# Performance work log

Hardware: AMD Instinct MI355X
Metric: run time of the kernel (lower is better)

The kernel has to match this reference:

```python
import jax, jax.numpy as jnp
import numpy as np

D_MODEL = 1024
N_HEADS = 16
N_KV_HEADS = 4
HEAD_DIM = D_MODEL // N_HEADS
GROUP = N_HEADS // N_KV_HEADS
ROPE_BASE = 10000.0


def _rope(x):
    # x: (B, H, T, Dh); standard rotate-half RoPE, base 10000
    B, H, T, Dh = x.shape
    inv_freq = 1.0 / (ROPE_BASE ** (jnp.arange(0, Dh, 2, dtype=jnp.float32) / Dh))
    t = jnp.arange(T, dtype=jnp.float32)
    freqs = t[:, None] * inv_freq[None, :]              # (T, Dh/2)
    emb = jnp.concatenate([freqs, freqs], axis=-1)      # (T, Dh)
    cos = jnp.cos(emb)[None, None].astype(x.dtype)
    sin = jnp.sin(emb)[None, None].astype(x.dtype)
    x1, x2 = x[..., : Dh // 2], x[..., Dh // 2 :]
    rot = jnp.concatenate([-x2, x1], axis=-1)
    return x * cos + rot * sin


def setup_inputs() -> dict:
    key = jax.random.key(0)
    ks = jax.random.split(key, 5)
    B, T = 2, 2048
    s = 1.0 / np.sqrt(D_MODEL)
    return {
        "x": jax.random.normal(ks[0], (B, T, D_MODEL), dtype=jnp.float32),
        "wq": jax.random.normal(ks[1], (D_MODEL, N_HEADS * HEAD_DIM), dtype=jnp.float32) * s,
        "wk": jax.random.normal(ks[2], (D_MODEL, N_KV_HEADS * HEAD_DIM), dtype=jnp.float32) * s,
        "wv": jax.random.normal(ks[3], (D_MODEL, N_KV_HEADS * HEAD_DIM), dtype=jnp.float32) * s,
        "wo": jax.random.normal(ks[4], (N_HEADS * HEAD_DIM, D_MODEL), dtype=jnp.float32) * s,
    }


def reference(x, wq, wk, wv, wo):
    B, T, _ = x.shape
    q = (x @ wq).reshape(B, T, N_HEADS, HEAD_DIM).transpose(0, 2, 1, 3)      # (B,H,T,Dh)
    k = (x @ wk).reshape(B, T, N_KV_HEADS, HEAD_DIM).transpose(0, 2, 1, 3)   # (B,Hk,T,Dh)
    v = (x @ wv).reshape(B, T, N_KV_HEADS, HEAD_DIM).transpose(0, 2, 1, 3)
    q = _rope(q)
    k = _rope(k)
    # repeat_interleave kv heads group_size times -> (B, H, T, Dh)
    k = jnp.repeat(k, GROUP, axis=1)
    v = jnp.repeat(v, GROUP, axis=1)
    scale = 1.0 / np.sqrt(HEAD_DIM)
    scores = jnp.einsum("bhqd,bhkd->bhqk", q, k) * scale                      # (B,H,T,T)
    causal = jnp.tril(jnp.ones((T, T), dtype=bool))
    scores = jnp.where(causal[None, None], scores, -jnp.inf)
    attn = jax.nn.softmax(scores, axis=-1)
    out = jnp.einsum("bhqk,bhkd->bhqd", attn, v)                              # (B,H,T,Dh)
    out = out.transpose(0, 2, 1, 3).reshape(B, T, N_HEADS * HEAD_DIM)
    return out @ wo
```

## Files before the change

### kernel.cpp

```cpp
#include <hip/hip_runtime.h>

typedef short bshort8 __attribute__((ext_vector_type(8)));
typedef float f32x4 __attribute__((ext_vector_type(4)));

#define DEVFN static __device__ __forceinline__

DEVFN unsigned short f2bf(float f) {
    union { float f; unsigned u; } v; v.f = f;
    unsigned r = (v.u + 0x7FFFu + ((v.u >> 16) & 1u)) >> 16;
    return (unsigned short)r;
}

DEVFN float bf2f(unsigned short u) {
    union { unsigned u; float f; } v; v.u = (unsigned)u << 16;
    return v.f;
}

DEVFN unsigned cvt_pk_bf16(float a, float b) {
    unsigned r;
    asm("v_cvt_pk_bf16_f32 %0, %1, %2" : "=v"(r) : "v"(a), "v"(b));
    return r;
}

DEVFN float exp2_fast(float x) {
    float r;
    asm("v_exp_f32 %0, %1" : "=v"(r) : "v"(x));
    return r;
}

DEVFN float max3f(float a, float b, float c) {
    float r;
    asm("v_max3_f32 %0, %1, %2, %3" : "=v"(r) : "v"(a), "v"(b), "v"(c));
    return r;
}

DEVFN int swzf(int row) { return (row & 7) ^ ((row >> 3) & 7); }
DEVFN int swzf2(int row) { return (row & 3) ^ ((row >> 2) & 3); }

#define GLDS16(g, l)                                                            \
    __builtin_amdgcn_global_load_lds(                                           \
        (__attribute__((address_space(1))) void*)(g),                           \
        (__attribute__((address_space(3))) void*)(l), 16, 0, 0)

__global__ void prep_kernel(const float* __restrict__ x,
                            const float* __restrict__ wq,
                            const float* __restrict__ wk,
                            const float* __restrict__ wv,
                            const float* __restrict__ wo,
                            unsigned short* __restrict__ xb,
                            unsigned short* __restrict__ wt,
                            unsigned short* __restrict__ wot,
                            float2* __restrict__ cs) {
    const int z = blockIdx.z;
    int tx = threadIdx.x, ty = threadIdx.y;
    if (z >= 5) {
        int i = ((z - 5) * 1024 + blockIdx.y * 32 + blockIdx.x) * 256 + ty * 32 + tx;
        float4 v = ((const float4*)x)[i];
        ushort4 o;
        o.x = f2bf(v.x); o.y = f2bf(v.y); o.z = f2bf(v.z); o.w = f2bf(v.w);
        ((ushort4*)xb)[i] = o;
        return;
    }
    if (z == 4) {
        int idx = (blockIdx.y * 32 + blockIdx.x) * 256 + ty * 32 + tx;
        if (idx < 65536) {
            int t = idx >> 5, i = idx & 31;
            float inv_freq = powf(10000.0f, -(float)i / 32.0f);
            float a = (float)t * inv_freq;
            cs[idx] = make_float2(cosf(a), sinf(a));
        }
        return;
    }
    const float* src;
    unsigned short* dst;
    int N;
    if (z == 0)      { src = wq; dst = wt;                N = 1024; }
    else if (z == 1) { src = wk; dst = wt + 1024 * 1024;  N = 256; }
    else if (z == 2) { src = wv; dst = wt + 1280 * 1024;  N = 256; }
    else             { src = wo; dst = wot;               N = 1024; }
    if (blockIdx.x * 32 >= N) return;
    __shared__ float tile[32][33];
    int n0 = blockIdx.x * 32, k0 = blockIdx.y * 32;
#pragma unroll
    for (int i = 0; i < 4; i++)
        tile[ty + i * 8][tx] = src[(size_t)(k0 + ty + i * 8) * N + n0 + tx];
    __syncthreads();
#pragma unroll
    for (int i = 0; i < 4; i++)
        dst[(size_t)(n0 + ty + i * 8) * 1024 + k0 + tx] = f2bf(tile[tx][ty + i * 8]);
}


__global__ __launch_bounds__(256) void gemm_qkv_kernel(
    const unsigned short* __restrict__ xb, const unsigned short* __restrict__ wt,
    const float2* __restrict__ cs, unsigned short* __restrict__ Qb,
    unsigned short* __restrict__ Kb, unsigned short* __restrict__ Vt) {
    __shared__ char smem[49152];
    const int tid = threadIdx.x;
    const int lane = tid & 63, w = tid >> 6;
    const int m0 = blockIdx.y * 128, n0 = blockIdx.x * 64;
    const int l15 = lane & 15, g = lane >> 4;
    const int l8 = lane >> 3, c8 = lane & 7;

    const unsigned short* srcA[4];
    int dstA[4];
#pragma unroll
    for (int j = 0; j < 4; j++) {
        int row = w * 32 + j * 8 + l8;
        srcA[j] = xb + (size_t)(m0 + row) * 1024 + (c8 ^ swzf(row)) * 8;
        dstA[j] = w * 4096 + j * 1024 + lane * 16;
    }
    const unsigned short* srcB[2];
    int dstB[2];
#pragma unroll
    for (int j = 0; j < 2; j++) {
        int row = w * 16 + j * 8 + l8;
        srcB[j] = wt + (size_t)(n0 + row) * 1024 + (c8 ^ swzf(row)) * 8;
        dstB[j] = 0x8000 + w * 2048 + j * 1024 + lane * 16;
    }

    int aOff[2][2], bOff[4][2];
#pragma unroll
    for (int fm = 0; fm < 2; fm++) {
        int row = w * 32 + fm * 16 + l15;
#pragma unroll
        for (int ks = 0; ks < 2; ks++)
            aOff[fm][ks] = row * 128 + (((ks * 4 + g) ^ swzf(row)) << 4);
    }
#pragma unroll
    for (int fn = 0; fn < 4; fn++) {
        int row = fn * 16 + l15;
#pragma unroll
        for (int ks = 0; ks < 2; ks++)
            bOff[fn][ks] = row * 128 + (((ks * 4 + g) ^ swzf(row)) << 4);
    }

    f32x4 acc[2][4] = {};
#pragma unroll
    for (int j = 0; j < 4; j++) GLDS16(srcA[j], smem + dstA[j]);
#pragma unroll
    for (int j = 0; j < 2; j++) GLDS16(srcB[j], smem + dstB[j]);
    asm volatile("s_waitcnt vmcnt(0)" ::: "memory");
    __builtin_amdgcn_s_barrier();

    for (int kt = 0; kt < 16; kt++) {
        const int curA = (kt & 1) << 14;
        const int curB = (kt & 1) << 13;
        if (kt < 15) {
            const int nA = curA ^ 0x4000, nB = curB ^ 0x2000;
#pragma unroll
            for (int j = 0; j < 4; j++)
                GLDS16(srcA[j] + (kt + 1) * 64, smem + nA + dstA[j]);
#pragma unroll
            for (int j = 0; j < 2; j++)
                GLDS16(srcB[j] + (kt + 1) * 64, smem + nB + dstB[j]);
        }
        bshort8 af[2][2], bf[4][2];
#pragma unroll
        for (int fm = 0; fm < 2; fm++)
#pragma unroll
            for (int ks = 0; ks < 2; ks++)
                af[fm][ks] = *(const bshort8*)(smem + curA + aOff[fm][ks]);
#pragma unroll
        for (int fn = 0; fn < 4; fn++)
#pragma unroll
            for (int ks = 0; ks < 2; ks++)
                bf[fn][ks] = *(const bshort8*)(smem + 0x8000 + curB + bOff[fn][ks]);
        asm volatile("s_waitcnt lgkmcnt(0)" ::: "memory");
        __builtin_amdgcn_sched_barrier(0);
#pragma unroll
        for (int fm = 0; fm < 2; fm++)
#pragma unroll
            for (int fn = 0; fn < 4; fn++) {
                acc[fm][fn] = __builtin_amdgcn_mfma_f32_16x16x32_bf16(
                    af[fm][0], bf[fn][0], acc[fm][fn], 0, 0, 0);
                acc[fm][fn] = __builtin_amdgcn_mfma_f32_16x16x32_bf16(
                    af[fm][1], bf[fn][1], acc[fm][fn], 0, 0, 0);
            }
        if (kt < 15) {
            asm volatile("s_waitcnt vmcnt(0)" ::: "memory");
            __builtin_amdgcn_s_barrier();
        }
    }

    const bool isV = (n0 >= 1280);
    const bool isK = (n0 >= 1024) && !isV;
#pragma unroll
    for (int fm = 0; fm < 2; fm++) {
#pragma unroll
        for (int r = 0; r < 4; r++) {
            int m = m0 + w * 32 + fm * 16 + g * 4 + r;
            int b = m >> 11, t = m & 2047;
            if (isV) {
#pragma unroll
                for (int fn = 0; fn < 4; fn++) {
                    int n = n0 + fn * 16 + l15;
                    int d = n & 63, vh = (n - 1280) >> 6;
                    Vt[((size_t)(b * 4 + vh) * 64 + d) * 2048 + t] =
                        f2bf(acc[fm][fn][r]);
                }
            } else {
                float2 c0 = cs[t * 32 + l15];
                float2 c1 = cs[t * 32 + 16 + l15];
#pragma unroll
                for (int fn = 0; fn < 4; fn++) {
                    int n = n0 + fn * 16 + l15;
                    int d = n & 63;
                    float val = acc[fm][fn][r];
                    float pair = acc[fm][fn ^ 2][r];
                    float rot = (fn < 2) ? -pair : pair;
                    float2 cc = (fn & 1) ? c1 : c0;
                    float o = val * cc.x + rot * cc.y;
                    if (isK) {
                        int kh = (n - 1024) >> 6;
                        Kb[((size_t)(b * 4 + kh) * 2048 + t) * 64 + d] = f2bf(o);
                    } else {
                        o *= 0.1803368801111504f;
                        int h = n >> 6;
                        Qb[((size_t)(b * 16 + h) * 2048 + t) * 64 + d] = f2bf(o);
                    }
                }
            }
        }
    }
}


__global__ __launch_bounds__(256) void attn_kernel(
    const unsigned short* __restrict__ Qb, const unsigned short* __restrict__ Kb,
    const unsigned short* __restrict__ Vt, unsigned short* __restrict__ Opart,
    float* __restrict__ ml) {
    __shared__ char smem[32768];
    const int tid = threadIdx.x, lane = tid & 63, w = tid >> 6;
    const int l15 = lane & 15, g = lane >> 4;
    const int id = blockIdx.x;
    const int grp = id & 7;
    const int b = grp >> 2, kvh = grp & 3;
    const int i = id >> 3;
    const int hh = i & 3;
    const int h = kvh * 4 + hh;
    const int c = 79 - (i >> 2);
    int qt, s;
    if (c < 8)       { qt = c;                    s = 0; }
    else if (c < 24) { qt = 8 + ((c - 8) >> 1);   s = (c - 8) & 1; }
    else if (c < 48) { qt = 16 + (c - 24) / 3;    s = (c - 24) % 3; }
    else             { qt = 24 + ((c - 48) >> 2); s = (c - 48) & 3; }
    const int k0t = s * 8;
    const int nk = min(8, qt + 1 - k0t);
    const int qs = qt * 64;
    const int slot = (b * 16 + h) * 80 + c;

    const unsigned short* Kbase = Kb + (size_t)(b * 4 + kvh) * 2048 * 64;
    const unsigned short* Vbase = Vt + (size_t)(b * 4 + kvh) * 64 * 2048;
    const unsigned short* Qhead = Qb + (size_t)(b * 16 + h) * 2048 * 64;

    const int srow8 = lane >> 3;
    const int sci = lane & 7;
    const int sk = (l15 & 7) ^ (l15 >> 3);
    const int strip = w * 2048;

    const int rowb = l15 * 128 + ((g ^ sk) << 4);
    const int Aq0 = strip + rowb;
    const int Ak0 = 0x2000 + rowb;
    const int Ak1 = Ak0 ^ 64;
    int Av0 = 0x4000 + rowb;
    int Av1 = Av0 ^ 64;
    const int pw0 = strip + l15 * 128 + (((2 * g) ^ sk) << 4);
    const int pw1 = strip + l15 * 128 + (((2 * g + 1) ^ sk) << 4);
    const int byteA0 = ((2 * g) & 3) * 32 + (g >> 1) * 8;
    const int byteB0 = ((2 * g + 1) & 3) * 32 + (g >> 1) * 8;
    const int prA0 = strip + l15 * 128 + (((byteA0 >> 4) ^ sk) << 4) + (byteA0 & 15);
    const int prB0 = strip + l15 * 128 + (((byteB0 >> 4) ^ sk) << 4) + (byteB0 & 15);

    const int lc0 = sci ^ srow8;
    const int lc1 = sci ^ srow8 ^ 1;
    const int r0 = w * 16 + srow8, r1 = w * 16 + 8 + srow8;
    const int kdst = 0x2000 + strip + lane * 16;
    int vdst = 0x4000 + strip + lane * 16;

    GLDS16(Qhead + (size_t)(qs + r0) * 64 + lc0 * 8, smem + strip + lane * 16);
    GLDS16(Qhead + (size_t)(qs + r1) * 64 + lc1 * 8, smem + strip + lane * 16 + 1024);
    GLDS16(Kbase + (size_t)(k0t * 64 + r0) * 64 + lc0 * 8, smem + kdst);
    GLDS16(Kbase + (size_t)(k0t * 64 + r1) * 64 + lc1 * 8, smem + kdst + 1024);
    GLDS16(Vbase + (size_t)r0 * 2048 + k0t * 64 + lc0 * 8, smem + vdst);
    GLDS16(Vbase + (size_t)r1 * 2048 + k0t * 64 + lc1 * 8, smem + vdst + 1024);
    __syncthreads();

    bshort8 qf0 = *(const bshort8*)(smem + Aq0);
    bshort8 qf1 = *(const bshort8*)(smem + (Aq0 ^ 64));
    bshort8 ones;
#pragma unroll
    for (int j = 0; j < 8; j++) ones[j] = (short)0x3F80;

    const unsigned short* gk0 = Kbase + (size_t)((k0t + 1) * 64 + r0) * 64 + lc0 * 8;
    const unsigned short* gk1 = Kbase + (size_t)((k0t + 1) * 64 + r1) * 64 + lc1 * 8;
    const unsigned short* gv0 = Vbase + (size_t)r0 * 2048 + (k0t + 1) * 64 + lc0 * 8;
    const unsigned short* gv1 = Vbase + (size_t)r1 * 2048 + (k0t + 1) * 64 + lc1 * 8;

    float m_run = -1e30f;
    f32x4 l_acc = {};
    f32x4 O[4] = {};
    const int qlocal = w * 16 + l15;

    for (int kt = 0; kt < nk; kt++) {
        if (kt < nk - 1) {
            GLDS16(gv0, smem + (vdst ^ 0x2000));
            GLDS16(gv1, smem + (vdst ^ 0x2000) + 1024);
            gv0 += 64; gv1 += 64;
        }
        f32x4 S[4];
        __builtin_amdgcn_s_setprio(1);
#pragma unroll
        for (int fn = 0; fn < 4; fn++) {
            bshort8 k0 = *(const bshort8*)(smem + Ak0 + fn * 2048);
            bshort8 k1 = *(const bshort8*)(smem + Ak1 + fn * 2048);
            f32x4 a = {};
            a = __builtin_amdgcn_mfma_f32_16x16x32_bf16(k0, qf0, a, 0, 0, 0);
            a = __builtin_amdgcn_mfma_f32_16x16x32_bf16(k1, qf1, a, 0, 0, 0);
            S[fn] = a;
        }
        __builtin_amdgcn_s_setprio(0);
        __builtin_amdgcn_s_barrier();
        if (kt < nk - 1) {
            GLDS16(gk0, smem + kdst);
            GLDS16(gk1, smem + kdst + 1024);
            gk0 += 4096; gk1 += 4096;
        }
        if (k0t + kt == qt) {
#pragma unroll
            for (int fn = 0; fn < 4; fn++)
#pragma unroll
                for (int r = 0; r < 4; r++)
                    if (fn * 16 + g * 4 + r > qlocal) S[fn][r] = -1e30f;
        }
        float ta = max3f(S[0][0], S[0][1], S[0][2]);
        float tb = max3f(S[0][3], S[1][0], S[1][1]);
        float tc = max3f(S[1][2], S[1][3], S[2][0]);
        float td = max3f(S[2][1], S[2][2], S[2][3]);
        float te = max3f(S[3][0], S[3][1], S[3][2]);
        float mt = fmaxf(max3f(ta, tb, tc), max3f(td, te, S[3][3]));
        mt = fmaxf(mt, __shfl_xor(mt, 16));
        mt = fmaxf(mt, __shfl_xor(mt, 32));
        if (!__all(mt <= m_run + 8.0f)) {
            float mn = fmaxf(m_run, mt);
            float alpha = exp2_fast(m_run - mn);
            m_run = mn;
            l_acc *= alpha;
#pragma unroll
            for (int fd = 0; fd < 4; fd++) O[fd] *= alpha;
        }
        float p[4][4];
#pragma unroll
        for (int fn = 0; fn < 4; fn++)
#pragma unroll
            for (int r = 0; r < 4; r++) p[fn][r] = exp2_fast(S[fn][r] - m_run);
        int4 w0v, w1v;
        w0v.x = cvt_pk_bf16(p[0][0], p[0][1]);
        w0v.y = cvt_pk_bf16(p[0][2], p[0][3]);
        w0v.z = cvt_pk_bf16(p[1][0], p[1][1]);
        w0v.w = cvt_pk_bf16(p[1][2], p[1][3]);
        w1v.x = cvt_pk_bf16(p[2][0], p[2][1]);
        w1v.y = cvt_pk_bf16(p[2][2], p[2][3]);
        w1v.z = cvt_pk_bf16(p[3][0], p[3][1]);
        w1v.w = cvt_pk_bf16(p[3][2], p[3][3]);
        *(int4*)(smem + pw0) = w0v;
        *(int4*)(smem + pw1) = w1v;
        asm volatile("s_waitcnt lgkmcnt(0)" ::: "memory");
        __builtin_amdgcn_sched_barrier(0);
        union PF { int2 d[2]; bshort8 v; };
        PF u0, u1;
        u0.d[0] = *(const int2*)(smem + prA0);
        u0.d[1] = *(const int2*)(smem + prB0);
        u1.d[0] = *(const int2*)(smem + (prA0 ^ 16));
        u1.d[1] = *(const int2*)(smem + (prB0 ^ 16));
        __builtin_amdgcn_s_setprio(1);
        l_acc = __builtin_amdgcn_mfma_f32_16x16x32_bf16(ones, u0.v, l_acc, 0, 0, 0);
        l_acc = __builtin_amdgcn_mfma_f32_16x16x32_bf16(ones, u1.v, l_acc, 0, 0, 0);
#pragma unroll
        for (int fd = 0; fd < 4; fd++) {
            bshort8 v0 = *(const bshort8*)(smem + Av0 + fd * 2048);
            bshort8 v1 = *(const bshort8*)(smem + Av1 + fd * 2048);
            O[fd] = __builtin_amdgcn_mfma_f32_16x16x32_bf16(v0, u0.v, O[fd], 0, 0, 0);
            O[fd] = __builtin_amdgcn_mfma_f32_16x16x32_bf16(v1, u1.v, O[fd], 0, 0, 0);
        }
        __builtin_amdgcn_s_setprio(0);
        Av0 ^= 0x2000; Av1 ^= 0x2000; vdst ^= 0x2000;
        if (kt < nk - 1) __syncthreads();
    }

    if (g == 0) {
        ((float2*)ml)[(size_t)slot * 64 + w * 16 + l15] =
            make_float2(m_run, l_acc[0]);
    }
#pragma unroll
    for (int fd = 0; fd < 4; fd++)
#pragma unroll
        for (int w2 = 0; w2 < 2; w2++) {
            unsigned word = cvt_pk_bf16(O[fd][2 * w2], O[fd][2 * w2 + 1]);
            int byte = fd * 32 + g * 8 + w2 * 4;
            *(unsigned*)(smem + strip + l15 * 128 + (((byte >> 4) ^ sk) << 4) +
                         (byte & 15)) = word;
        }
    asm volatile("s_waitcnt lgkmcnt(0)" ::: "memory");
    __builtin_amdgcn_sched_barrier(0);
#pragma unroll
    for (int it = 0; it < 2; it++) {
        int r16 = it * 8 + srow8;
        int4 vv = *(const int4*)(smem + strip + r16 * 128 +
                                 ((sci ^ srow8 ^ it) << 4));
        *(int4*)(Opart + (size_t)slot * 4096 + (w * 16 + r16) * 64 + sci * 8) = vv;
    }
}

__global__ __launch_bounds__(256) void combine_kernel(
    const unsigned short* __restrict__ Opart, const float* __restrict__ ml,
    unsigned short* __restrict__ Ob) {
    const int qt = blockIdx.x, h = blockIdx.y, b = blockIdx.z;
    const int S = (qt >> 3) + 1;
    int c0;
    if (qt < 8)       c0 = qt;
    else if (qt < 16) c0 = 8 + (qt - 8) * 2;
    else if (qt < 24) c0 = 24 + (qt - 16) * 3;
    else              c0 = 48 + (qt - 24) * 4;
    const int slotbase = (b * 16 + h) * 80 + c0;
    const int t = threadIdx.x;
    const int q = t >> 2, dq = (t & 3) * 16;
    const float2* ml2 = (const float2*)ml;

    float m[4], l[4];
    float mstar = -1e30f;
#pragma unroll
    for (int i = 0; i < 4; i++) {
        m[i] = -1e30f; l[i] = 0.f;
        if (i < S) {
            float2 v = ml2[(size_t)(slotbase + i) * 64 + q];
            m[i] = v.x; l[i] = v.y;
            mstar = fmaxf(mstar, v.x);
        }
    }
    float L = 0.f;
    float wgt[4];
#pragma unroll
    for (int i = 0; i < 4; i++) {
        wgt[i] = (i < S) ? exp2f(m[i] - mstar) : 0.f;
        L += wgt[i] * l[i];
    }
    float acc[16] = {};
#pragma unroll
    for (int i = 0; i < 4; i++) {
        if (i < S) {
            const unsigned short* P =
                Opart + (size_t)(slotbase + i) * 4096 + q * 64 + dq;
            int4 a0 = *(const int4*)P;
            int4 a1 = *(const int4*)(P + 8);
            unsigned u[8] = {(unsigned)a0.x, (unsigned)a0.y, (unsigned)a0.z,
                             (unsigned)a0.w, (unsigned)a1.x, (unsigned)a1.y,
                             (unsigned)a1.z, (unsigned)a1.w};
            float wi = wgt[i];
#pragma unroll
            for (int j = 0; j < 8; j++) {
                acc[2 * j]     += wi * bf2f((unsigned short)(u[j] & 0xFFFF));
                acc[2 * j + 1] += wi * bf2f((unsigned short)(u[j] >> 16));
            }
        }
    }
    float invL = 1.0f / L;
    int4 o0, o1;
    o0.x = cvt_pk_bf16(acc[0] * invL, acc[1] * invL);
    o0.y = cvt_pk_bf16(acc[2] * invL, acc[3] * invL);
    o0.z = cvt_pk_bf16(acc[4] * invL, acc[5] * invL);
    o0.w = cvt_pk_bf16(acc[6] * invL, acc[7] * invL);
    o1.x = cvt_pk_bf16(acc[8] * invL, acc[9] * invL);
    o1.y = cvt_pk_bf16(acc[10] * invL, acc[11] * invL);
    o1.z = cvt_pk_bf16(acc[12] * invL, acc[13] * invL);
    o1.w = cvt_pk_bf16(acc[14] * invL, acc[15] * invL);
    unsigned short* dst =
        Ob + (size_t)(b * 2048 + qt * 64 + q) * 1024 + h * 64 + dq;
    *(int4*)dst = o0;
    *(int4*)(dst + 8) = o1;
}

__global__ __launch_bounds__(256) void gemm_out_kernel(
    const unsigned short* __restrict__ ab, const unsigned short* __restrict__ wot,
    float* __restrict__ out) {
    __shared__ char smem[49152];
    const int tid = threadIdx.x;
    const int lane = tid & 63, w = tid >> 6;
    const int m0 = blockIdx.y * 128, n0 = blockIdx.x * 64;
    const int l15 = lane & 15, g = lane >> 4;
    const int l8 = lane >> 3, c8 = lane & 7;

    const unsigned short* srcA[4];
    int dstA[4];
#pragma unroll
    for (int j = 0; j < 4; j++) {
        int row = w * 32 + j * 8 + l8;
        srcA[j] = ab + (size_t)(m0 + row) * 1024 + (c8 ^ swzf(row)) * 8;
        dstA[j] = w * 4096 + j * 1024 + lane * 16;
    }
    const unsigned short* srcB[2];
    int dstB[2];
#pragma unroll
    for (int j = 0; j < 2; j++) {
        int row = w * 16 + j * 8 + l8;
        srcB[j] = wot + (size_t)(n0 + row) * 1024 + (c8 ^ swzf(row)) * 8;
        dstB[j] = 0x8000 + w * 2048 + j * 1024 + lane * 16;
    }

    int aOff[2][2], bOff[4][2];
#pragma unroll
    for (int fm = 0; fm < 2; fm++) {
        int row = w * 32 + fm * 16 + l15;
#pragma unroll
        for (int ks = 0; ks < 2; ks++)
            aOff[fm][ks] = row * 128 + (((ks * 4 + g) ^ swzf(row)) << 4);
    }
#pragma unroll
    for (int fn = 0; fn < 4; fn++) {
        int row = fn * 16 + l15;
#pragma unroll
        for (int ks = 0; ks < 2; ks++)
            bOff[fn][ks] = row * 128 + (((ks * 4 + g) ^ swzf(row)) << 4);
    }

    f32x4 acc[2][4] = {};
#pragma unroll
    for (int j = 0; j < 4; j++) GLDS16(srcA[j], smem + dstA[j]);
#pragma unroll
    for (int j = 0; j < 2; j++) GLDS16(srcB[j], smem + dstB[j]);
    asm volatile("s_waitcnt vmcnt(0)" ::: "memory");
    __builtin_amdgcn_s_barrier();

    for (int kt = 0; kt < 16; kt++) {
        const int curA = (kt & 1) << 14;
        const int curB = (kt & 1) << 13;
        if (kt < 15) {
            const int nA = curA ^ 0x4000, nB = curB ^ 0x2000;
#pragma unroll
            for (int j = 0; j < 4; j++)
                GLDS16(srcA[j] + (kt + 1) * 64, smem + nA + dstA[j]);
#pragma unroll
            for (int j = 0; j < 2; j++)
                GLDS16(srcB[j] + (kt + 1) * 64, smem + nB + dstB[j]);
        }
        bshort8 af[2][2], bf[4][2];
#pragma unroll
        for (int fm = 0; fm < 2; fm++)
#pragma unroll
            for (int ks = 0; ks < 2; ks++)
                af[fm][ks] = *(const bshort8*)(smem + curA + aOff[fm][ks]);
#pragma unroll
        for (int fn = 0; fn < 4; fn++)
#pragma unroll
            for (int ks = 0; ks < 2; ks++)
                bf[fn][ks] = *(const bshort8*)(smem + 0x8000 + curB + bOff[fn][ks]);
        asm volatile("s_waitcnt lgkmcnt(0)" ::: "memory");
        __builtin_amdgcn_sched_barrier(0);
#pragma unroll
        for (int fm = 0; fm < 2; fm++)
#pragma unroll
            for (int fn = 0; fn < 4; fn++) {
                acc[fm][fn] = __builtin_amdgcn_mfma_f32_16x16x32_bf16(
                    af[fm][0], bf[fn][0], acc[fm][fn], 0, 0, 0);
                acc[fm][fn] = __builtin_amdgcn_mfma_f32_16x16x32_bf16(
                    af[fm][1], bf[fn][1], acc[fm][fn], 0, 0, 0);
            }
        if (kt < 15) {
            asm volatile("s_waitcnt vmcnt(0)" ::: "memory");
            __builtin_amdgcn_s_barrier();
        }
    }
#pragma unroll
    for (int fm = 0; fm < 2; fm++)
#pragma unroll
        for (int r = 0; r < 4; r++) {
            int m = m0 + w * 32 + fm * 16 + g * 4 + r;
#pragma unroll
            for (int fn = 0; fn < 4; fn++) {
                int n = n0 + fn * 16 + l15;
                out[(size_t)m * 1024 + n] = acc[fm][fn][r];
            }
        }
}


extern "C" void kernel_launch(void* const* d_in, const int* in_sizes, int n_in,
                              void* d_out, int out_size, void* d_ws, size_t ws_size,
                              hipStream_t stream) {
    const float* x = (const float*)d_in[0];
    const float* wq = (const float*)d_in[1];
    const float* wk = (const float*)d_in[2];
    const float* wv = (const float*)d_in[3];
    const float* wo = (const float*)d_in[4];
    float* out = (float*)d_out;
    char* ws = (char*)d_ws;

    unsigned short* xb = (unsigned short*)(ws);
    unsigned short* wt = (unsigned short*)(ws + 8388608);
    float* ml = (float*)(ws + 8388608);
    unsigned short* wot = (unsigned short*)(ws + 11534336);
    float2* cs = (float2*)(ws + 13631488);
    unsigned short* Qb = (unsigned short*)(ws + 14155776);
    unsigned short* Kb = (unsigned short*)(ws + 22544384);
    unsigned short* Vtr = (unsigned short*)(ws + 26738688);
    unsigned short* Opart = (unsigned short*)(ws + 28835840);
    unsigned short* Ob = xb;

    hipLaunchKernelGGL(prep_kernel, dim3(32, 32, 9), dim3(32, 8), 0, stream, x,
                       wq, wk, wv, wo, xb, wt, wot, cs);
    hipLaunchKernelGGL(gemm_qkv_kernel, dim3(24, 32), dim3(256), 0, stream, xb, wt,
                       cs, Qb, Kb, Vtr);
    hipLaunchKernelGGL(attn_kernel, dim3(2560), dim3(256), 0, stream, Qb, Kb,
                       Vtr, Opart, ml);
    hipLaunchKernelGGL(combine_kernel, dim3(32, 16, 2), dim3(256), 0, stream,
                       Opart, ml, Ob);
    hipLaunchKernelGGL(gemm_out_kernel, dim3(16, 32), dim3(256), 0, stream, Ob,
                       wot, out);
}
```

Baseline: 97.85 us.

## Permute K row mapping so P stays in registers for PV MFMA

Reorders which K rows each S-tile MFMA reads, so that the MFMA output layout of the score tile directly matches the B-operand layout needed for the P·V MFMA. This removes the round trip through shared memory (bf16 stores, an lgkmcnt wait, a scheduling barrier and scattered reloads) for the probability matrix on every KV tile. The causal mask index is rewritten to match the new permutation, and K reads now use per-fragment precomputed addresses with a different swizzle key, which may change the bank-conflict behaviour of those reads.

```diff
diff --git a/kernel.cpp b/kernel.cpp
--- a/kernel.cpp
+++ b/kernel.cpp
@@ -261,16 +261,15 @@
 
     const int rowb = l15 * 128 + ((g ^ sk) << 4);
     const int Aq0 = strip + rowb;
-    const int Ak0 = 0x2000 + rowb;
-    const int Ak1 = Ak0 ^ 64;
+    int Akn[4];
+#pragma unroll
+    for (int fn = 0; fn < 4; fn++) {
+        int nr = ((fn >> 1) << 5) + ((l15 >> 2) << 3) + ((fn & 1) << 2) + (l15 & 3);
+        int key = (nr & 7) ^ ((nr >> 3) & 1);
+        Akn[fn] = 0x2000 + nr * 128 + ((g ^ key) << 4);
+    }
     int Av0 = 0x4000 + rowb;
     int Av1 = Av0 ^ 64;
-    const int pw0 = strip + l15 * 128 + (((2 * g) ^ sk) << 4);
-    const int pw1 = strip + l15 * 128 + (((2 * g + 1) ^ sk) << 4);
-    const int byteA0 = ((2 * g) & 3) * 32 + (g >> 1) * 8;
-    const int byteB0 = ((2 * g + 1) & 3) * 32 + (g >> 1) * 8;
-    const int prA0 = strip + l15 * 128 + (((byteA0 >> 4) ^ sk) << 4) + (byteA0 & 15);
-    const int prB0 = strip + l15 * 128 + (((byteB0 >> 4) ^ sk) << 4) + (byteB0 & 15);
 
     const int lc0 = sci ^ srow8;
     const int lc1 = sci ^ srow8 ^ 1;
@@ -312,8 +311,8 @@
         __builtin_amdgcn_s_setprio(1);
 #pragma unroll
         for (int fn = 0; fn < 4; fn++) {
-            bshort8 k0 = *(const bshort8*)(smem + Ak0 + fn * 2048);
-            bshort8 k1 = *(const bshort8*)(smem + Ak1 + fn * 2048);
+            bshort8 k0 = *(const bshort8*)(smem + Akn[fn]);
+            bshort8 k1 = *(const bshort8*)(smem + (Akn[fn] ^ 0x40));
             f32x4 a = {};
             a = __builtin_amdgcn_mfma_f32_16x16x32_bf16(k0, qf0, a, 0, 0, 0);
             a = __builtin_amdgcn_mfma_f32_16x16x32_bf16(k1, qf1, a, 0, 0, 0);
@@ -330,8 +329,10 @@
 #pragma unroll
             for (int fn = 0; fn < 4; fn++)
 #pragma unroll
-                for (int r = 0; r < 4; r++)
-                    if (fn * 16 + g * 4 + r > qlocal) S[fn][r] = -1e30f;
+                for (int r = 0; r < 4; r++) {
+                    int kvl = ((fn >> 1) << 5) + (g << 3) + ((fn & 1) << 2) + r;
+                    if (kvl > qlocal) S[fn][r] = -1e30f;
+                }
         }
         float ta = max3f(S[0][0], S[0][1], S[0][2]);
         float tb = max3f(S[0][3], S[1][0], S[1][1]);
@@ -354,25 +355,16 @@
         for (int fn = 0; fn < 4; fn++)
 #pragma unroll
             for (int r = 0; r < 4; r++) p[fn][r] = exp2_fast(S[fn][r] - m_run);
-        int4 w0v, w1v;
-        w0v.x = cvt_pk_bf16(p[0][0], p[0][1]);
-        w0v.y = cvt_pk_bf16(p[0][2], p[0][3]);
-        w0v.z = cvt_pk_bf16(p[1][0], p[1][1]);
-        w0v.w = cvt_pk_bf16(p[1][2], p[1][3]);
-        w1v.x = cvt_pk_bf16(p[2][0], p[2][1]);
-        w1v.y = cvt_pk_bf16(p[2][2], p[2][3]);
-        w1v.z = cvt_pk_bf16(p[3][0], p[3][1]);
-        w1v.w = cvt_pk_bf16(p[3][2], p[3][3]);
-        *(int4*)(smem + pw0) = w0v;
-        *(int4*)(smem + pw1) = w1v;
-        asm volatile("s_waitcnt lgkmcnt(0)" ::: "memory");
-        __builtin_amdgcn_sched_barrier(0);
-        union PF { int2 d[2]; bshort8 v; };
+        union PF { unsigned d[4]; bshort8 v; };
         PF u0, u1;
-        u0.d[0] = *(const int2*)(smem + prA0);
-        u0.d[1] = *(const int2*)(smem + prB0);
-        u1.d[0] = *(const int2*)(smem + (prA0 ^ 16));
-        u1.d[1] = *(const int2*)(smem + (prB0 ^ 16));
+        u0.d[0] = cvt_pk_bf16(p[0][0], p[0][1]);
+        u0.d[1] = cvt_pk_bf16(p[0][2], p[0][3]);
+        u0.d[2] = cvt_pk_bf16(p[1][0], p[1][1]);
+        u0.d[3] = cvt_pk_bf16(p[1][2], p[1][3]);
+        u1.d[0] = cvt_pk_bf16(p[2][0], p[2][1]);
+        u1.d[1] = cvt_pk_bf16(p[2][2], p[2][3]);
+        u1.d[2] = cvt_pk_bf16(p[3][0], p[3][1]);
+        u1.d[3] = cvt_pk_bf16(p[3][2], p[3][3]);
         __builtin_amdgcn_s_setprio(1);
         l_acc = __builtin_amdgcn_mfma_f32_16x16x32_bf16(ones, u0.v, l_acc, 0, 0, 0);
         l_acc = __builtin_amdgcn_mfma_f32_16x16x32_bf16(ones, u1.v, l_acc, 0, 0, 0);
```

After: 94.74 us, median of 2. 3.2% less time.
